# Kernel optimization log

Measured on AMD Instinct MI355X. Metric: run time of the kernel, lower is better.

The kernel has to match this reference:

```python
import jax, jax.numpy as jnp
import numpy as np

BLOCK_SIZE = 2048
FRAMES = 4096
BASE_RESONANCE = 0.5
MAX_GAIN = 5.0


def fft_convolve(a, b):
    # Linear convolution via zero-padded FFT, truncated to original length
    # (matches the matching-pursuit repo's fft_convolve).
    n = a.shape[-1]
    fa = jnp.fft.rfft(a, n=2 * n, axis=-1)
    fb = jnp.fft.rfft(b, n=2 * n, axis=-1)
    out = jnp.fft.irfft(fa * fb, n=2 * n, axis=-1)
    return out[..., :n]


def setup_inputs() -> dict:
    key = jax.random.key(0)
    ks = jax.random.split(key, 6)
    cp = jax.random.normal(ks[0], (1, BLOCK_SIZE, FRAMES), dtype=jnp.float32)
    w1 = jax.random.uniform(ks[1], (BLOCK_SIZE, BLOCK_SIZE), jnp.float32, -0.01, 0.01)
    w2 = jax.random.uniform(ks[2], (BLOCK_SIZE, BLOCK_SIZE), jnp.float32, -0.01, 0.01)
    audio = jax.random.uniform(ks[3], (BLOCK_SIZE, BLOCK_SIZE), jnp.float32, -0.01, 0.01)
    decays = jax.random.uniform(ks[4], (BLOCK_SIZE,), jnp.float32, 0.001, 0.99)
    gains = jax.random.uniform(ks[5], (BLOCK_SIZE,), jnp.float32, -3.0, 3.0)
    return {"cp": cp, "w1": w1, "w2": w2, "audio": audio, "decays": decays, "gains": gains}


def reference(cp, w1, w2, audio, decays, gains):
    b, c, frames = cp.shape  # b == 1, c == BLOCK_SIZE
    x0 = jnp.maximum(cp, 0.0)  # torch.relu(cp)
    # decay values in (base_resonance, 1): base + sigmoid(decays) * span
    d = BASE_RESONANCE + jax.nn.sigmoid(decays) * (1.0 - BASE_RESONANCE)  # (c,)
    g = jax.nn.sigmoid(gains) * MAX_GAIN  # (c,)

    x = jnp.einsum('ij,bjt->bit', w1, x0)  # mapping @ control_plane
    orig = x

    # decay envelope: log -> cumsum -> exp over frames => d ** (t+1)
    logd = jnp.log(1e-12 + jnp.broadcast_to(d[None, :, None], (b, c, frames)))
    denv = jnp.exp(jnp.cumsum(logd, axis=-1))  # (b, c, frames)

    x = fft_convolve(x, denv)
    x = jnp.einsum('ij,bjt->bit', w2, x) + orig
    cp_out = jnp.tanh(x * g[None, :, None])

    audio_out = jnp.einsum('wj,bjt->bwt', audio, cp_out)  # (b, window, frames)
    audio_out = jnp.transpose(audio_out, (0, 2, 1)).reshape(b, 1, -1)
    return audio_out, cp_out
```

## Files before the change

kernel.cpp:

```cpp
#include <hip/hip_runtime.h>
#include <math.h>

typedef __attribute__((ext_vector_type(8))) short bf16x8;
typedef __attribute__((ext_vector_type(8))) unsigned short u16x8;
typedef __attribute__((ext_vector_type(4))) unsigned short u16x4;
typedef __attribute__((ext_vector_type(4))) float f32x4;
typedef unsigned short u16;

__device__ __forceinline__ u16 f2bf(float f) {
  unsigned u = __builtin_bit_cast(unsigned, f);
  return (u16)((u + 0x7FFFu + ((u >> 16) & 1u)) >> 16);
}

__device__ __forceinline__ void gload16(const u16* g, u16* l) {
  __builtin_amdgcn_global_load_lds((const __attribute__((address_space(1))) void*)g,
                                   (__attribute__((address_space(3))) void*)l, 16, 0, 0);
}

__device__ __forceinline__ void sbar() {
  __builtin_amdgcn_sched_barrier(0);
  __builtin_amdgcn_s_barrier();
  __builtin_amdgcn_sched_barrier(0);
}

#define VMWAIT(n) asm volatile("s_waitcnt vmcnt(" #n ")" ::: "memory")
#define MFMA16(a, b, c) __builtin_amdgcn_mfma_f32_16x16x32_bf16((a), (b), (c), 0, 0, 0)

__device__ __forceinline__ float decay_of(float d) {
  return 1e-12f + 0.5f + 0.5f / (1.0f + expf(-d));
}

__device__ __forceinline__ size_t pack_idx(int nrow, int k) {
  const int bn = nrow >> 7, n16 = (nrow >> 4) & 7, row = nrow & 15;
  const int kt = k >> 6, kh = (k >> 5) & 1, kc = (k >> 3) & 3;
  return ((((size_t)(bn * 32 + kt) * 8 + n16) * 2 + kh) * 4 + kc) * 16 + row;
}

__global__ __launch_bounds__(256) void cvt2_kernel(const float* __restrict__ a,
                                                   const float* __restrict__ b,
                                                   u16* __restrict__ out) {
  const int i = blockIdx.x * 256 + threadIdx.x;
  const float* src = (i < 1048576) ? a : b;
  const int j = (i < 1048576) ? i : i - 1048576;
  const float4 v = ((const float4*)src)[j];
  u16x4 o = { f2bf(v.x), f2bf(v.y), f2bf(v.z), f2bf(v.w) };
  ((u16x4*)out)[i] = o;
}

__global__ __launch_bounds__(256) void audio_pack_kernel(const float* __restrict__ audio,
                                                         u16* __restrict__ pack) {
  const int gid = blockIdx.x * 256 + threadIdx.x;
  const int j = (gid & 255) * 8;
  const int wv = gid >> 8;
  const float4 v0 = *(const float4*)(audio + (size_t)wv * 2048 + j);
  const float4 v1 = *(const float4*)(audio + (size_t)wv * 2048 + j + 4);
  u16x8 o = { f2bf(v0.x), f2bf(v0.y), f2bf(v0.z), f2bf(v0.w),
              f2bf(v1.x), f2bf(v1.y), f2bf(v1.z), f2bf(v1.w) };
  *(u16x8*)(pack + pack_idx(wv, j) * 8) = o;
}

__global__ __launch_bounds__(256) void relu_t_kernel(const float* __restrict__ cp,
                                                     u16* __restrict__ x0p) {
  const int cb = blockIdx.x & 31;
  const int tb = blockIdx.x >> 5;
  __shared__ __attribute__((aligned(16))) float tile[64][65];
  const int tid = threadIdx.x;
  const int r0 = tid >> 4, i4 = (tid & 15) * 4;
  #pragma unroll
  for (int rr = 0; rr < 64; rr += 16) {
    const float4 v = *(const float4*)(cp + (size_t)(cb * 64 + r0 + rr) * 4096 + tb * 64 + i4);
    tile[r0 + rr][i4 + 0] = fmaxf(v.x, 0.f);
    tile[r0 + rr][i4 + 1] = fmaxf(v.y, 0.f);
    tile[r0 + rr][i4 + 2] = fmaxf(v.z, 0.f);
    tile[r0 + rr][i4 + 3] = fmaxf(v.w, 0.f);
  }
  __syncthreads();
  #pragma unroll
  for (int it = 0; it < 2; ++it) {
    const int chunk = it * 256 + tid;
    const int i = chunk >> 3, rp = (chunk & 7) * 8;
    u16x8 o;
    #pragma unroll
    for (int q = 0; q < 8; ++q) o[q] = f2bf(tile[rp + q][i]);
    *(u16x8*)(x0p + pack_idx(tb * 64 + i, cb * 64 + rp) * 8) = o;
  }
}

__global__ __launch_bounds__(128) void iir_partial_kernel(const float* __restrict__ x,
                                                          const float* __restrict__ decays,
                                                          float* __restrict__ L) {
  const int tid = threadIdx.x;
  const int cb = blockIdx.x & 15;
  const int ck = blockIdx.x >> 4;
  const int c0 = cb * 128, t0 = ck * 64;
  __shared__ __attribute__((aligned(16))) float xs[128][65];
  const float dd = decay_of(decays[c0 + tid]);
  #pragma unroll
  for (int it = 0; it < 16; ++it) {
    const int idx = it * 128 + tid;
    const int r = idx >> 4, iv = (idx & 15) * 4;
    const float4 v = *(const float4*)(x + (size_t)(c0 + r) * 4096 + t0 + iv);
    xs[r][iv + 0] = v.x; xs[r][iv + 1] = v.y; xs[r][iv + 2] = v.z; xs[r][iv + 3] = v.w;
  }
  __syncthreads();
  float yv = 0.0f;
  #pragma unroll
  for (int i = 0; i < 64; ++i) yv = dd * (xs[tid][i] + yv);
  L[ck * 2048 + c0 + tid] = yv;
}

__global__ __launch_bounds__(128) void iir_carry_kernel(const float* __restrict__ L,
                                                        const float* __restrict__ decays,
                                                        float* __restrict__ Cin) {
  const int c = blockIdx.x * 128 + threadIdx.x;
  const float dd = decay_of(decays[c]);
  float A = dd;
  #pragma unroll
  for (int p = 0; p < 6; ++p) A = A * A;
  float carry = 0.0f;
  for (int j = 0; j < 64; ++j) {
    Cin[j * 2048 + c] = carry;
    carry = L[j * 2048 + c] + A * carry;
  }
}

__global__ __launch_bounds__(128) void iir_apply_kernel(const float* __restrict__ x,
                                                        const float* __restrict__ decays,
                                                        const float* __restrict__ Cin,
                                                        u16* __restrict__ yp) {
  const int tid = threadIdx.x;
  const int cb = blockIdx.x & 15;
  const int ck = blockIdx.x >> 4;
  const int c0 = cb * 128, t0 = ck * 64;
  __shared__ __attribute__((aligned(16))) float xs[128][65];
  __shared__ __attribute__((aligned(16))) u16 ys[64][136];
  const float dd = decay_of(decays[c0 + tid]);
  const float carry = Cin[ck * 2048 + c0 + tid];
  #pragma unroll
  for (int it = 0; it < 16; ++it) {
    const int idx = it * 128 + tid;
    const int r = idx >> 4, iv = (idx & 15) * 4;
    const float4 v = *(const float4*)(x + (size_t)(c0 + r) * 4096 + t0 + iv);
    xs[r][iv + 0] = v.x; xs[r][iv + 1] = v.y; xs[r][iv + 2] = v.z; xs[r][iv + 3] = v.w;
  }
  __syncthreads();
  float yv = carry;
  #pragma unroll
  for (int i = 0; i < 64; ++i) {
    yv = dd * (xs[tid][i] + yv);
    ys[i][tid] = f2bf(yv);
  }
  __syncthreads();
  #pragma unroll
  for (int it = 0; it < 8; ++it) {
    const int chunk = it * 128 + tid;
    const int i = chunk >> 4, cpv = (chunk & 15) * 8;
    u16x8 v = *(const u16x8*)&ys[i][cpv];
    *(u16x8*)(yp + pack_idx(t0 + i, c0 + cpv) * 8) = v;
  }
}

template <int MODE>
__global__ __launch_bounds__(256, 2) void gemm_rr_kernel(
    const u16* __restrict__ A, const u16* __restrict__ Bp, float* __restrict__ C,
    int N, int K, int xlogn,
    const float* __restrict__ orig, const float* __restrict__ gains,
    u16* __restrict__ CbT) {
  __shared__ __attribute__((aligned(16))) u16 Asb[2][128 * 64];
  const int tid = threadIdx.x;
  const int l = tid & 63, w = tid >> 6;
  const int xc = blockIdx.x & 7, rblk = blockIdx.x >> 3;
  const int xn = xc & ((1 << xlogn) - 1), xm = xc >> xlogn;
  const int bm = xm * 8 + (rblk >> 3);
  const int bn = xn * 8 + (rblk & 7);
  const int nt = K >> 6;

  const int cs = (l & 7) ^ (l >> 3);
  const int rsub = l >> 3;
  const u16* aS[4]; int tO[4];
  #pragma unroll
  for (int u = 0; u < 4; ++u) {
    const int rg = (u * 4 + w) * 8 + rsub;
    aS[u] = A + (size_t)(bm * 128 + rg) * K + cs * 8;
    tO[u] = (u * 4 + w) * 512;
  }

#define STAGEA(buf, tt) do {                                               \
    const long so_ = (long)(tt) * 64;                                      \
    gload16(aS[0] + so_, (buf) + tO[0]); gload16(aS[1] + so_, (buf) + tO[1]); \
    gload16(aS[2] + so_, (buf) + tO[2]); gload16(aS[3] + so_, (buf) + tO[3]); \
  } while (0)

  const int wr = w >> 1, wc = w & 1;
  const int rA0 = wr * 64 + (l & 15);
  const int jk0 = (l >> 4) ^ (l & 7);
  const int jk1 = ((l >> 4) + 4) ^ (l & 7);

  const u16* bBase = Bp + ((size_t)bn * nt * 8 + wc * 4) * 1024 + (size_t)l * 8;

#define LOADB(dst, tt) do {                                                \
    const u16* bp_ = bBase + (size_t)(tt) * 8192;                          \
    dst[0][0] = *(const bf16x8*)(bp_ +    0); dst[0][1] = *(const bf16x8*)(bp_ +  512); \
    dst[1][0] = *(const bf16x8*)(bp_ + 1024); dst[1][1] = *(const bf16x8*)(bp_ + 1536); \
    dst[2][0] = *(const bf16x8*)(bp_ + 2048); dst[2][1] = *(const bf16x8*)(bp_ + 2560); \
    dst[3][0] = *(const bf16x8*)(bp_ + 3072); dst[3][1] = *(const bf16x8*)(bp_ + 3584); \
  } while (0)

#define READA(dst, Ab) do {                                                \
    _Pragma("unroll")                                                      \
    for (int mi = 0; mi < 4; ++mi) {                                       \
      dst[mi][0] = *(const bf16x8*)((Ab) + (rA0 + mi * 16) * 64 + jk0 * 8);\
      dst[mi][1] = *(const bf16x8*)((Ab) + (rA0 + mi * 16) * 64 + jk1 * 8);\
    }                                                                      \
  } while (0)

#define COMPUTE(afr, bfr) do {                                             \
    __builtin_amdgcn_s_setprio(1);                                         \
    _Pragma("unroll")                                                      \
    for (int mi = 0; mi < 4; ++mi)                                         \
      _Pragma("unroll")                                                    \
      for (int ni = 0; ni < 4; ++ni)                                       \
        acc[mi][ni] = MFMA16(afr[mi][0], bfr[ni][0], acc[mi][ni]);         \
    _Pragma("unroll")                                                      \
    for (int mi = 0; mi < 4; ++mi)                                         \
      _Pragma("unroll")                                                    \
      for (int ni = 0; ni < 4; ++ni)                                       \
        acc[mi][ni] = MFMA16(afr[mi][1], bfr[ni][1], acc[mi][ni]);         \
    __builtin_amdgcn_s_setprio(0);                                         \
  } while (0)

  f32x4 acc[4][4];
  #pragma unroll
  for (int i = 0; i < 4; ++i)
    #pragma unroll
    for (int j = 0; j < 4; ++j) acc[i][j] = (f32x4){0.f, 0.f, 0.f, 0.f};

  bf16x8 aE[4][2], aO[4][2], bfE[4][2], bfO[4][2];
  u16* Asb0 = (u16*)Asb[0];
  u16* Asb1 = (u16*)Asb[1];

  STAGEA(Asb0, 0);
  LOADB(bfE, 0);
  STAGEA(Asb1, 1);
  VMWAIT(12);
  sbar();
  READA(aE, Asb0);

  for (int t = 0; t < nt; t += 2) {
    const bool m2 = (t + 2) < nt;
    LOADB(bfO, t + 1);
    VMWAIT(12);
    COMPUTE(aE, bfE);
    VMWAIT(8);
    sbar();
    if (m2) STAGEA(Asb0, t + 2);
    READA(aO, Asb1);
    if (m2) LOADB(bfE, t + 2);
    if (m2) { VMWAIT(12); } else { VMWAIT(0); }
    COMPUTE(aO, bfO);
    if (m2) {
      VMWAIT(8);
      sbar();
      STAGEA(Asb1, t + 3);
      READA(aE, Asb0);
    }
  }
#undef STAGEA
#undef LOADB
#undef READA
#undef COMPUTE

  const int rb = bm * 128 + wr * 64 + ((l >> 4) * 4);
  const int cb = bn * 128 + wc * 64 + (l & 15);
  #pragma unroll
  for (int mi = 0; mi < 4; ++mi) {
    const int row0 = rb + mi * 16;
    float gv[4] = {0.f, 0.f, 0.f, 0.f};
    if (MODE == 1) {
      #pragma unroll
      for (int j = 0; j < 4; ++j) gv[j] = 5.0f / (1.0f + expf(-gains[row0 + j]));
    }
    #pragma unroll
    for (int ni = 0; ni < 4; ++ni) {
      const int col = cb + ni * 16;
      f32x4 v = acc[mi][ni];
      if (MODE == 1) {
        float cpv[4];
        #pragma unroll
        for (int j = 0; j < 4; ++j) {
          float t = v[j] + orig[(size_t)(row0 + j) * N + col];
          cpv[j] = tanhf(t * gv[j]);
          C[(size_t)(row0 + j) * N + col] = cpv[j];
        }
        u16x4 o = { f2bf(cpv[0]), f2bf(cpv[1]), f2bf(cpv[2]), f2bf(cpv[3]) };
        *(u16x4*)(CbT + (size_t)col * 2048 + row0) = o;
      } else {
        #pragma unroll
        for (int j = 0; j < 4; ++j)
          C[(size_t)(row0 + j) * N + col] = v[j];
      }
    }
  }
}

extern "C" void kernel_launch(void* const* d_in, const int* in_sizes, int n_in,
                              void* d_out, int out_size, void* d_ws, size_t ws_size,
                              hipStream_t stream) {
  const float* cp     = (const float*)d_in[0];
  const float* w1     = (const float*)d_in[1];
  const float* w2     = (const float*)d_in[2];
  const float* audio  = (const float*)d_in[3];
  const float* decays = (const float*)d_in[4];
  const float* gains  = (const float*)d_in[5];

  float* out0 = (float*)d_out;
  float* out1 = out0 + (size_t)2048 * 4096;

  char* ws = (char*)d_ws;
  u16*   w1b    = (u16*)(ws);
  u16*   w2b    = (u16*)(ws + 8388608);
  u16*   audp   = (u16*)(ws + 16777216);
  float* orig   = (float*)(ws + 25165824);
  u16*   yp     = (u16*)(ws + 58720256);
  u16*   x0p    = (u16*)(ws + 75497472);
  u16*   cpbT   = x0p;
  float* Lbuf   = (float*)(ws + 75497472);
  float* Cin    = (float*)(ws + 75497472 + 524288);

  cvt2_kernel<<<8192, 256, 0, stream>>>(w1, w2, w1b);
  audio_pack_kernel<<<2048, 256, 0, stream>>>(audio, audp);
  relu_t_kernel<<<2048, 256, 0, stream>>>(cp, x0p);

  gemm_rr_kernel<0><<<512, 256, 0, stream>>>(w1b, x0p, orig, 4096, 2048, 2,
                                             nullptr, nullptr, nullptr);
  iir_partial_kernel<<<1024, 128, 0, stream>>>(orig, decays, Lbuf);
  iir_carry_kernel<<<16, 128, 0, stream>>>(Lbuf, decays, Cin);
  iir_apply_kernel<<<1024, 128, 0, stream>>>(orig, decays, Cin, yp);
  gemm_rr_kernel<1><<<512, 256, 0, stream>>>(w2b, yp, out1, 4096, 2048, 2,
                                             orig, gains, cpbT);
  gemm_rr_kernel<0><<<512, 256, 0, stream>>>(cpbT, audp, out0, 2048, 2048, 1,
                                             nullptr, nullptr, nullptr);
}
```

Measured before the change: 200.3 us.

## Halve GEMM N-tile to 64 and raise occupancy to four blocks per CU

Result: no change. 201.6 us (+0.6%).

```diff
diff --git a/kernel.cpp b/kernel.cpp
--- a/kernel.cpp
+++ b/kernel.cpp
@@ -161,7 +161,7 @@
 }
 
 template <int MODE>
-__global__ __launch_bounds__(256, 2) void gemm_rr_kernel(
+__global__ __launch_bounds__(256, 4) void gemm_n64_kernel(
     const u16* __restrict__ A, const u16* __restrict__ Bp, float* __restrict__ C,
     int N, int K, int xlogn,
     const float* __restrict__ orig, const float* __restrict__ gains,
@@ -171,8 +171,8 @@
   const int l = tid & 63, w = tid >> 6;
   const int xc = blockIdx.x & 7, rblk = blockIdx.x >> 3;
   const int xn = xc & ((1 << xlogn) - 1), xm = xc >> xlogn;
-  const int bm = xm * 8 + (rblk >> 3);
-  const int bn = xn * 8 + (rblk & 7);
+  const int bm = xm * 8 + (rblk >> 4);
+  const int bn = xn * 16 + (rblk & 15);
   const int nt = K >> 6;
 
   const int cs = (l & 7) ^ (l >> 3);
@@ -196,82 +196,75 @@
   const int jk0 = (l >> 4) ^ (l & 7);
   const int jk1 = ((l >> 4) + 4) ^ (l & 7);
 
-  const u16* bBase = Bp + ((size_t)bn * nt * 8 + wc * 4) * 1024 + (size_t)l * 8;
+  const u16* bBase = Bp + ((size_t)(bn >> 1) * 256 + (bn & 1) * 4 + wc * 2) * 1024
+                        + (size_t)l * 8;
 
 #define LOADB(dst, tt) do {                                                \
     const u16* bp_ = bBase + (size_t)(tt) * 8192;                          \
     dst[0][0] = *(const bf16x8*)(bp_ +    0); dst[0][1] = *(const bf16x8*)(bp_ +  512); \
     dst[1][0] = *(const bf16x8*)(bp_ + 1024); dst[1][1] = *(const bf16x8*)(bp_ + 1536); \
-    dst[2][0] = *(const bf16x8*)(bp_ + 2048); dst[2][1] = *(const bf16x8*)(bp_ + 2560); \
-    dst[3][0] = *(const bf16x8*)(bp_ + 3072); dst[3][1] = *(const bf16x8*)(bp_ + 3584); \
   } while (0)
 
-#define READA(dst, Ab) do {                                                \
+#define COMPUTE(Ab, bfr) do {                                              \
+    bf16x8 af[4][2];                                                       \
     _Pragma("unroll")                                                      \
     for (int mi = 0; mi < 4; ++mi) {                                       \
-      dst[mi][0] = *(const bf16x8*)((Ab) + (rA0 + mi * 16) * 64 + jk0 * 8);\
-      dst[mi][1] = *(const bf16x8*)((Ab) + (rA0 + mi * 16) * 64 + jk1 * 8);\
+      af[mi][0] = *(const bf16x8*)((Ab) + (rA0 + mi * 16) * 64 + jk0 * 8); \
+      af[mi][1] = *(const bf16x8*)((Ab) + (rA0 + mi * 16) * 64 + jk1 * 8); \
     }                                                                      \
-  } while (0)
-
-#define COMPUTE(afr, bfr) do {                                             \
     __builtin_amdgcn_s_setprio(1);                                         \
     _Pragma("unroll")                                                      \
     for (int mi = 0; mi < 4; ++mi)                                         \
       _Pragma("unroll")                                                    \
-      for (int ni = 0; ni < 4; ++ni)                                       \
-        acc[mi][ni] = MFMA16(afr[mi][0], bfr[ni][0], acc[mi][ni]);         \
+      for (int ni = 0; ni < 2; ++ni)                                       \
+        acc[mi][ni] = MFMA16(af[mi][0], bfr[ni][0], acc[mi][ni]);          \
     _Pragma("unroll")                                                      \
     for (int mi = 0; mi < 4; ++mi)                                         \
       _Pragma("unroll")                                                    \
-      for (int ni = 0; ni < 4; ++ni)                                       \
-        acc[mi][ni] = MFMA16(afr[mi][1], bfr[ni][1], acc[mi][ni]);         \
+      for (int ni = 0; ni < 2; ++ni)                                       \
+        acc[mi][ni] = MFMA16(af[mi][1], bfr[ni][1], acc[mi][ni]);          \
     __builtin_amdgcn_s_setprio(0);                                         \
   } while (0)
 
-  f32x4 acc[4][4];
+  f32x4 acc[4][2];
   #pragma unroll
   for (int i = 0; i < 4; ++i)
     #pragma unroll
-    for (int j = 0; j < 4; ++j) acc[i][j] = (f32x4){0.f, 0.f, 0.f, 0.f};
-
-  bf16x8 aE[4][2], aO[4][2], bfE[4][2], bfO[4][2];
+    for (int j = 0; j < 2; ++j) acc[i][j] = (f32x4){0.f, 0.f, 0.f, 0.f};
+
+  bf16x8 bfE[2][2], bfO[2][2];
   u16* Asb0 = (u16*)Asb[0];
   u16* Asb1 = (u16*)Asb[1];
 
   STAGEA(Asb0, 0);
   LOADB(bfE, 0);
   STAGEA(Asb1, 1);
-  VMWAIT(12);
+  VMWAIT(8);
   sbar();
-  READA(aE, Asb0);
 
   for (int t = 0; t < nt; t += 2) {
     const bool m2 = (t + 2) < nt;
     LOADB(bfO, t + 1);
-    VMWAIT(12);
-    COMPUTE(aE, bfE);
     VMWAIT(8);
+    COMPUTE(Asb0, bfE);
+    VMWAIT(4);
     sbar();
     if (m2) STAGEA(Asb0, t + 2);
-    READA(aO, Asb1);
-    if (m2) LOADB(bfE, t + 2);
-    if (m2) { VMWAIT(12); } else { VMWAIT(0); }
-    COMPUTE(aO, bfO);
+    if (m2) { LOADB(bfE, t + 2); VMWAIT(8); }
+    else    { VMWAIT(0); }
+    COMPUTE(Asb1, bfO);
     if (m2) {
-      VMWAIT(8);
+      VMWAIT(4);
       sbar();
       STAGEA(Asb1, t + 3);
-      READA(aE, Asb0);
     }
   }
 #undef STAGEA
 #undef LOADB
-#undef READA
 #undef COMPUTE
 
   const int rb = bm * 128 + wr * 64 + ((l >> 4) * 4);
-  const int cb = bn * 128 + wc * 64 + (l & 15);
+  const int cb = bn * 64 + wc * 32 + (l & 15);
   #pragma unroll
   for (int mi = 0; mi < 4; ++mi) {
     const int row0 = rb + mi * 16;
@@ -281,7 +274,7 @@
       for (int j = 0; j < 4; ++j) gv[j] = 5.0f / (1.0f + expf(-gains[row0 + j]));
     }
     #pragma unroll
-    for (int ni = 0; ni < 4; ++ni) {
+    for (int ni = 0; ni < 2; ++ni) {
       const int col = cb + ni * 16;
       f32x4 v = acc[mi][ni];
       if (MODE == 1) {
@@ -331,13 +324,13 @@
   audio_pack_kernel<<<2048, 256, 0, stream>>>(audio, audp);
   relu_t_kernel<<<2048, 256, 0, stream>>>(cp, x0p);
 
-  gemm_rr_kernel<0><<<512, 256, 0, stream>>>(w1b, x0p, orig, 4096, 2048, 2,
-                                             nullptr, nullptr, nullptr);
+  gemm_n64_kernel<0><<<1024, 256, 0, stream>>>(w1b, x0p, orig, 4096, 2048, 2,
+                                               nullptr, nullptr, nullptr);
   iir_partial_kernel<<<1024, 128, 0, stream>>>(orig, decays, Lbuf);
   iir_carry_kernel<<<16, 128, 0, stream>>>(Lbuf, decays, Cin);
   iir_apply_kernel<<<1024, 128, 0, stream>>>(orig, decays, Cin, yp);
-  gemm_rr_kernel<1><<<512, 256, 0, stream>>>(w2b, yp, out1, 4096, 2048, 2,
-                                             orig, gains, cpbT);
-  gemm_rr_kernel<0><<<512, 256, 0, stream>>>(cpbT, audp, out0, 2048, 2048, 1,
-                                             nullptr, nullptr, nullptr);
-}
+  gemm_n64_kernel<1><<<1024, 256, 0, stream>>>(w2b, yp, out1, 4096, 2048, 2,
+                                               orig, gains, cpbT);
+  gemm_n64_kernel<0><<<1024, 256, 0, stream>>>(cpbT, audp, out0, 2048, 2048, 1,
+                                               nullptr, nullptr, nullptr);
+}
```
